# Kernel tuning notes

Hardware: AMD Instinct MI355X
Metric: run time of the kernel (lower is better)

## Reference

```python
import jax, jax.numpy as jnp
import numpy as np

B, N, M = 2, 512, 8192
DIM, CTX, H, DH, MULT = 1024, 512, 16, 64, 4
INNER = H * DH


def layernorm(x, scale, bias, eps=1e-5):
    mu = x.mean(-1, keepdims=True)
    var = ((x - mu) ** 2).mean(-1, keepdims=True)
    return (x - mu) / jnp.sqrt(var + eps) * scale + bias


def rotate_half(x):
    # interleaved pairs: (..., d) -> (..., d/2, 2), (x1, x2) -> (-x2, x1)
    xr = x.reshape(x.shape[:-1] + (-1, 2))
    x1, x2 = xr[..., 0], xr[..., 1]
    return jnp.stack((-x2, x1), axis=-1).reshape(x.shape)


def apply_rope(freqs, x):
    # freqs: [b, seq, dh] -> [b, 1, seq, dh]; x: [b, h, seq, dh]
    f = freqs[:, None, :, :]
    return x * jnp.cos(f) + rotate_half(x) * jnp.sin(f)


def setup_inputs() -> dict:
    key = jax.random.key(0)
    ks = jax.random.split(key, 24)
    s = 0.02
    inp = {
        "x_query": jax.random.normal(ks[0], (B, N, DIM), jnp.float32),
        "x_context": jax.random.normal(ks[1], (B, M, CTX), jnp.float32),
        "rope_q": jax.random.normal(ks[2], (B, N, DH), jnp.float32),
        "rope_ctx": jax.random.normal(ks[3], (B, M, DH), jnp.float32),
        "Wq": jax.random.normal(ks[4], (DIM, INNER), jnp.float32) * s,
        "Wkv": jax.random.normal(ks[5], (CTX, 2 * INNER), jnp.float32) * s,
        "Wo": jax.random.normal(ks[6], (INNER, DIM), jnp.float32) * s,
        "bo": jnp.zeros((DIM,), jnp.float32),
        "ln_q_scale": jnp.ones((DIM,), jnp.float32),
        "ln_q_bias": jnp.zeros((DIM,), jnp.float32),
        "ln_c_scale": jnp.ones((CTX,), jnp.float32),
        "ln_c_bias": jnp.zeros((CTX,), jnp.float32),
        "ffn_ln_scale": jnp.ones((DIM,), jnp.float32),
        "ffn_ln_bias": jnp.zeros((DIM,), jnp.float32),
        "W1": jax.random.normal(ks[7], (DIM, DIM * MULT * 2), jnp.float32) * s,
        "b1": jnp.zeros((DIM * MULT * 2,), jnp.float32),
        "W2": jax.random.normal(ks[8], (DIM * MULT, DIM), jnp.float32) * s,
        "b2": jnp.zeros((DIM,), jnp.float32),
        "attn_mask": jnp.ones((B, M), dtype=bool),
    }
    return inp


def reference(x_query, x_context, rope_q, rope_ctx, Wq, Wkv, Wo, bo,
              ln_q_scale, ln_q_bias, ln_c_scale, ln_c_bias,
              ffn_ln_scale, ffn_ln_bias, W1, b1, W2, b2, attn_mask):
    # --- RotaryCrossAttention ---
    hq = layernorm(x_query, ln_q_scale, ln_q_bias)
    hc = layernorm(x_context, ln_c_scale, ln_c_bias)
    q = (hq @ Wq).reshape(B, N, H, DH).transpose(0, 2, 1, 3)          # b h n d
    kv = hc @ Wkv
    k = kv[..., :INNER].reshape(B, M, H, DH).transpose(0, 2, 1, 3)    # b h m d
    v = kv[..., INNER:].reshape(B, M, H, DH).transpose(0, 2, 1, 3)
    q = apply_rope(rope_q, q)
    k = apply_rope(rope_ctx, k)
    v = apply_rope(rope_ctx, v)  # rotate_value=True
    scale = DH ** -0.5
    scores = jnp.einsum('bhnd,bhmd->bhnm', q, k) * scale
    scores = jnp.where(attn_mask[:, None, None, :], scores, -1e9)
    attn = jax.nn.softmax(scores, axis=-1)
    out = jnp.einsum('bhnm,bhmd->bhnd', attn, v)
    out = apply_rope(-rope_q, out)  # un-rotate values
    out = out.transpose(0, 2, 1, 3).reshape(B, N, INNER)
    out = out @ Wo + bo
    res = x_query + out
    # --- pre-norm GEGLU FeedForward ---
    y = layernorm(res, ffn_ln_scale, ffn_ln_bias)
    u = y @ W1 + b1
    a, g = u[..., :DIM * MULT], u[..., DIM * MULT:]
    z = (a * jax.nn.gelu(g, approximate=False)) @ W2 + b2
    return res + z
```

## Files before the change

### kernel.cpp

```cpp
#include <hip/hip_runtime.h>
#include <hip/hip_bf16.h>
#include <math.h>


typedef __bf16 bf16;
typedef __bf16 bf16x8 __attribute__((ext_vector_type(8)));
typedef float f32x4 __attribute__((ext_vector_type(4)));

#define DEVI static __device__ __forceinline__

union BV {
  uint4 u;
  bf16 b[8];
  bf16x8 v;
};

DEVI float bf2f(bf16 x) { return (float)x; }
DEVI bf16 f2bf(float x) { return (bf16)x; }

DEVI void gload16(const void* g, void* l) {
  __builtin_amdgcn_global_load_lds((const __attribute__((address_space(1))) void*)g,
                                   (__attribute__((address_space(3))) void*)l, 16, 0, 0);
}

template <int EPI>
__global__ __launch_bounds__(256, 2)
void gemm128(const bf16* __restrict__ A, const bf16* __restrict__ Bt,
             int Mdim, int Ndim, int Kdim,
             const float* __restrict__ bias, const float* __restrict__ resid,
             void* __restrict__ out0, void* __restrict__ out1, int sshift) {
  extern __shared__ char smem[];
  bf16* As = (bf16*)smem;
  bf16* Bs = (bf16*)(smem + 16384);
  const int tid = threadIdx.x;
  const int w = tid >> 6, l = tid & 63;
  const int wm = w >> 1, wn = w & 1;
  const int ln15 = l & 15, lh = l >> 4;
  const int sw7 = ln15 & 7;
  int bm, bn;
  if constexpr (EPI == 5) {
    const int fid = blockIdx.x;
    bn = (fid & 7) * 16 + ((fid >> 3) & 15);
    bm = fid >> 7;
  } else {
    bm = blockIdx.x;
    bn = blockIdx.y;
  }
  const int kpz = Kdim / gridDim.z;
  const int kbeg = blockIdx.z * kpz;

  const int srow = w * 32 + (l >> 3);
  const int gcol = ((l & 7) ^ ((l >> 3) & 7)) << 3;
  const bf16* aG = A + (size_t)(bm * 128 + srow) * Kdim + gcol;
  const bf16* bG = Bt + (size_t)(bn * 128 + srow) * Kdim + gcol;
  bf16* lA = As + (w * 32) * 64;
  bf16* lB = Bs + (w * 32) * 64;

  const f32x4 z4 = {0.f, 0.f, 0.f, 0.f};
  f32x4 acc[4][4];
#pragma unroll
  for (int i = 0; i < 4; i++)
#pragma unroll
    for (int j = 0; j < 4; j++) acc[i][j] = z4;

  const char* Ab = (const char*)As;
  const char* Bb = (const char*)Bs;
  const int arow_b = (wm * 64 + ln15) * 128;
  const int brow_b = (wn * 64 + ln15) * 128;

  for (int k0 = kbeg; k0 < kbeg + kpz; k0 += 64) {
#pragma unroll
    for (int gi = 0; gi < 4; gi++) {
      gload16(aG + (size_t)(gi * 8) * Kdim + k0, lA + gi * 512);
      gload16(bG + (size_t)(gi * 8) * Kdim + k0, lB + gi * 512);
    }
    __syncthreads();
#pragma unroll
    for (int kk = 0; kk < 2; kk++) {
      const int gx = (((kk << 2) | lh) ^ sw7) << 4;
      bf16x8 af[4], bfr[4];
#pragma unroll
      for (int f = 0; f < 4; f++) {
        BV t0;
        t0.u = *(const uint4*)(Ab + arow_b + f * 2048 + gx);
        af[f] = t0.v;
        BV t2;
        t2.u = *(const uint4*)(Bb + brow_b + f * 2048 + gx);
        bfr[f] = t2.v;
      }
#pragma unroll
      for (int fm = 0; fm < 4; fm++)
#pragma unroll
        for (int fn = 0; fn < 4; fn++)
          acc[fm][fn] = __builtin_amdgcn_mfma_f32_16x16x32_bf16(af[fm], bfr[fn], acc[fm][fn], 0, 0, 0);
    }
    __syncthreads();
  }

  if constexpr (EPI == 5) {
    const unsigned* cs = (const unsigned*)resid;
    char* ot = smem;
    const bool isK = (bm < 8);
#pragma unroll
    for (int fm = 0; fm < 4; fm++) {
      const int nl0 = wm * 64 + fm * 16 + lh * 4;
#pragma unroll
      for (int fn = 0; fn < 4; fn++) {
        const int ml = wn * 64 + fn * 16 + ln15;
        const int col = bn * 128 + ml;
#pragma unroll
        for (int jp = 0; jp < 2; jp++) {
          const int nl = nl0 + 2 * jp;
          const int d0 = nl & 63;
          const float x0 = acc[fm][fn][2 * jp];
          const float x1 = acc[fm][fn][2 * jp + 1];
          const unsigned cs0 = cs[(size_t)d0 * 16384 + col];
          const unsigned cs1 = cs[(size_t)(d0 + 1) * 16384 + col];
          const float c0 = __uint_as_float(cs0 << 16);
          const float s0 = __uint_as_float(cs0 & 0xffff0000u);
          const float c1 = __uint_as_float(cs1 << 16);
          const float s1 = __uint_as_float(cs1 & 0xffff0000u);
          const float y0 = x0 * c0 - x1 * s0;
          const float y1 = x1 * c1 + x0 * s1;
          if (isK) {
            union { unsigned u; bf16 bb[2]; } pk;
            pk.bb[0] = f2bf(y0);
            pk.bb[1] = f2bf(y1);
            *(unsigned*)(ot + ml * 272 + nl * 2) = pk.u;
          } else {
            *(bf16*)(ot + nl * 272 + ml * 2) = f2bf(y0);
            *(bf16*)(ot + (nl + 1) * 272 + ml * 2) = f2bf(y1);
          }
        }
      }
    }
    __syncthreads();
    const int b = bn >> 6;
    const int mblk = (bn & 63) * 128;
    if (isK) {
#pragma unroll
      for (int it = 0; it < 8; it++) {
        const int id = it * 256 + tid;
        const int hl = id >> 10, rem = id & 1023;
        const int mm = rem >> 3, c = rem & 7;
        const uint4 vv = *(const uint4*)(ot + mm * 272 + hl * 128 + c * 16);
        const int hg = bm * 2 + hl;
        *(uint4*)((bf16*)out0 + ((size_t)(b * 16 + hg) * 8192 + mblk + mm) * 64 + c * 8) = vv;
      }
    } else {
#pragma unroll
      for (int it = 0; it < 8; it++) {
        const int id = it * 256 + tid;
        const int nl = id >> 4, c = id & 15;
        const uint4 vv = *(const uint4*)(ot + nl * 272 + c * 16);
        const int hg = (bm - 8) * 2 + (nl >> 6);
        const int d = nl & 63;
        *(uint4*)((bf16*)out1 + ((size_t)(b * 16 + hg) * 64 + d) * 8192 + mblk + c * 8) = vv;
      }
    }
  } else {
#pragma unroll
    for (int fm = 0; fm < 4; fm++) {
#pragma unroll
      for (int fn = 0; fn < 4; fn++) {
        const int col = bn * 128 + wn * 64 + fn * 16 + ln15;
#pragma unroll
        for (int j = 0; j < 4; j++) {
          const int row = bm * 128 + wm * 64 + fm * 16 + lh * 4 + j;
          if constexpr (EPI == 6) {
            ((bf16*)out0)[((size_t)blockIdx.z * Mdim + row) * Ndim + col] = f2bf(acc[fm][fn][j]);
          } else {
            ((float*)out0)[((size_t)blockIdx.z * Mdim + row) * Ndim + col] = acc[fm][fn][j];
          }
        }
      }
    }
  }
}

__global__ __launch_bounds__(256, 2)
void gemm_geglu(const bf16* __restrict__ A, const bf16* __restrict__ Bt,
                const float* __restrict__ b1, bf16* __restrict__ hg) {
  __shared__ bf16 As[128 * 64];
  __shared__ bf16 Bs[128 * 64];
  const int tid = threadIdx.x;
  const int w = tid >> 6, l = tid & 63;
  const int wm = w >> 1, wn = w & 1;
  const int bm = blockIdx.x, bn = blockIdx.y;
  const int ln15 = l & 15, lh = l >> 4;
  const int sw7 = ln15 & 7;

  const int srow = w * 32 + (l >> 3);
  const int gcol = ((l & 7) ^ ((l >> 3) & 7)) << 3;
  const bf16* aG = A + (size_t)(bm * 128 + srow) * 1024 + gcol;
  const bf16* bG = Bt + (size_t)((w >> 1) * 4096 + bn * 64 + ((w & 1) * 32 + (l >> 3))) * 1024 + gcol;
  bf16* lA = As + (w * 32) * 64;
  bf16* lB = Bs + (w * 32) * 64;

  const f32x4 z4 = {0.f, 0.f, 0.f, 0.f};
  f32x4 acc[2][4][2];
#pragma unroll
  for (int p = 0; p < 2; p++)
#pragma unroll
    for (int i = 0; i < 4; i++)
#pragma unroll
      for (int j = 0; j < 2; j++) acc[p][i][j] = z4;

  const char* Ab = (const char*)As;
  const char* Bb = (const char*)Bs;
  const int arow_b = (wm * 64 + ln15) * 128;

  for (int k0 = 0; k0 < 1024; k0 += 64) {
#pragma unroll
    for (int gi = 0; gi < 4; gi++) {
      gload16(aG + (size_t)(gi * 8) * 1024 + k0, lA + gi * 512);
      gload16(bG + (size_t)(gi * 8) * 1024 + k0, lB + gi * 512);
    }
    __syncthreads();
#pragma unroll
    for (int kk = 0; kk < 2; kk++) {
      const int gx = (((kk << 2) | lh) ^ sw7) << 4;
      bf16x8 af[4], bfr[2][2];
#pragma unroll
      for (int f = 0; f < 4; f++) {
        BV t0;
        t0.u = *(const uint4*)(Ab + arow_b + f * 2048 + gx);
        af[f] = t0.v;
      }
#pragma unroll
      for (int p = 0; p < 2; p++)
#pragma unroll
        for (int fn = 0; fn < 2; fn++) {
          BV t0;
          t0.u = *(const uint4*)(Bb + (p * 64 + wn * 32 + fn * 16 + ln15) * 128 + gx);
          bfr[p][fn] = t0.v;
        }
#pragma unroll
      for (int fm = 0; fm < 4; fm++)
#pragma unroll
        for (int p = 0; p < 2; p++)
#pragma unroll
          for (int fn = 0; fn < 2; fn++)
            acc[p][fm][fn] = __builtin_amdgcn_mfma_f32_16x16x32_bf16(af[fm], bfr[p][fn], acc[p][fm][fn], 0, 0, 0);
    }
    __syncthreads();
  }

#pragma unroll
  for (int fm = 0; fm < 4; fm++) {
#pragma unroll
    for (int fn = 0; fn < 2; fn++) {
      const int cl = bn * 64 + wn * 32 + fn * 16 + ln15;
      const float ba = b1[cl], bg = b1[4096 + cl];
#pragma unroll
      for (int j = 0; j < 4; j++) {
        const int row = bm * 128 + wm * 64 + fm * 16 + lh * 4 + j;
        const float a = acc[0][fm][fn][j] + ba;
        const float g = acc[1][fm][fn][j] + bg;
        const float ge = 0.5f * g * (1.f + erff(g * 0.70710678118f));
        hg[(size_t)row * 4096 + cl] = f2bf(a * ge);
      }
    }
  }
}

template <int S>
__global__ __launch_bounds__(256)
void combine_q_rope(const float* __restrict__ part, const float* __restrict__ ct_,
                    const float* __restrict__ st_, bf16* __restrict__ q_buf) {
  const size_t i4 = ((size_t)blockIdx.x * 256 + threadIdx.x) * 4;
  float4 s = *(const float4*)(part + i4);
#pragma unroll
  for (int p = 1; p < S; p++) {
    const float4 t = *(const float4*)(part + (size_t)p * 1048576 + i4);
    s.x += t.x; s.y += t.y; s.z += t.z; s.w += t.w;
  }
  const int row = (int)(i4 >> 10), col = (int)(i4 & 1023);
  const int h = col >> 6, d = col & 63;
  const int b = row >> 9, n = row & 511;
  const size_t fo = (((size_t)(b << 9) + n) << 6) + d;
  const float4 cv = *(const float4*)(ct_ + fo);
  const float4 sv = *(const float4*)(st_ + fo);
  const float SC = 0.125f * 1.44269504f;
  union { uint2 u; bf16 bb[4]; } o;
  o.bb[0] = f2bf((s.x * cv.x - s.y * sv.x) * SC);
  o.bb[1] = f2bf((s.y * cv.y + s.x * sv.y) * SC);
  o.bb[2] = f2bf((s.z * cv.z - s.w * sv.z) * SC);
  o.bb[3] = f2bf((s.w * cv.w + s.z * sv.w) * SC);
  *(uint2*)(q_buf + ((((size_t)(b * 16 + h)) << 9) + n) * 64 + d) = o.u;
}

template <int S>
__global__ __launch_bounds__(256)
void combine_res_kernel(const float* __restrict__ part, const float* __restrict__ bias,
                        const float* __restrict__ resid, float* __restrict__ out) {
  const size_t i4 = ((size_t)blockIdx.x * 256 + threadIdx.x) * 4;
  float4 s = *(const float4*)(part + i4);
#pragma unroll
  for (int p = 1; p < S; p++) {
    const float4 t = *(const float4*)(part + (size_t)p * 1048576 + i4);
    s.x += t.x; s.y += t.y; s.z += t.z; s.w += t.w;
  }
  const int col = (int)(i4 & 1023);
  const float4 bv = *(const float4*)(bias + col);
  const float4 rv = *(const float4*)(resid + i4);
  s.x += bv.x + rv.x; s.y += bv.y + rv.y; s.z += bv.z + rv.z; s.w += bv.w + rv.w;
  *(float4*)(out + i4) = s;
}

template <int S>
__global__ __launch_bounds__(256)
void combine_res_bf16(const bf16* __restrict__ part, const float* __restrict__ bias,
                      const float* __restrict__ resid, float* __restrict__ out) {
  const size_t i4 = ((size_t)blockIdx.x * 256 + threadIdx.x) * 4;
  float4 s = {0.f, 0.f, 0.f, 0.f};
#pragma unroll
  for (int p = 0; p < S; p++) {
    union { uint2 u; bf16 bb[4]; } t;
    t.u = *(const uint2*)(part + (size_t)p * 1048576 + i4);
    s.x += bf2f(t.bb[0]); s.y += bf2f(t.bb[1]);
    s.z += bf2f(t.bb[2]); s.w += bf2f(t.bb[3]);
  }
  const int col = (int)(i4 & 1023);
  const float4 bv = *(const float4*)(bias + col);
  const float4 rv = *(const float4*)(resid + i4);
  s.x += bv.x + rv.x; s.y += bv.y + rv.y; s.z += bv.z + rv.z; s.w += bv.w + rv.w;
  *(float4*)(out + i4) = s;
}

__global__ __launch_bounds__(256, 4)
void attn_kernel(const bf16* __restrict__ q_buf, const bf16* __restrict__ k_buf,
                 const bf16* __restrict__ v_t, bf16* __restrict__ opart,
                 float* __restrict__ lpart) {
  __shared__ bf16 Ks[2][64 * 64];
  __shared__ bf16 Vs[2][64 * 64];
  __shared__ bf16 Ps[4][16][64];
  const int id = blockIdx.x;
  const int sp = id >> 7, qt = (id >> 5) & 3, bh = id & 31;
  const int tid = threadIdx.x;
  const int w = tid >> 6, l = tid & 63;
  const int ln15 = l & 15, lh = l >> 4;

  const bf16* qbase = q_buf + ((size_t)bh * 512 + qt * 128 + w * 32) * 64;
  const bf16* kbase = k_buf + (size_t)bh * 8192 * 64;
  const bf16* vbase = v_t + (size_t)bh * 64 * 8192;

  bf16x8 aq[2][2];
#pragma unroll
  for (int rh = 0; rh < 2; rh++) {
    const bf16* qp = qbase + (size_t)(rh * 16 + ln15) * 64 + lh * 8;
    BV t0; t0.u = *(const uint4*)qp; aq[rh][0] = t0.v;
    BV t1; t1.u = *(const uint4*)(qp + 32); aq[rh][1] = t1.v;
  }

  const f32x4 z4 = {0.f, 0.f, 0.f, 0.f};
  f32x4 o[2][4];
#pragma unroll
  for (int rh = 0; rh < 2; rh++)
#pragma unroll
    for (int fd = 0; fd < 4; fd++) o[rh][fd] = z4;
  f32x4 ol[2] = {z4, z4};

  BV ones;
#pragma unroll
  for (int i = 0; i < 8; i++) ones.b[i] = f2bf(1.0f);

  const int srow0 = ((w << 1) | 0) * 8 + (l >> 3);
  const int srow1 = ((w << 1) | 1) * 8 + (l >> 3);
  const int slot = l & 7;
  const int g0 = (slot ^ (srow0 & 7)) << 3;
  const int g1 = (slot ^ (srow1 & 7)) << 3;
  const bf16* k0p = kbase + (size_t)srow0 * 64 + g0;
  const bf16* k1p = kbase + (size_t)srow1 * 64 + g1;
  const bf16* v0p = vbase + (size_t)srow0 * 8192 + g0;
  const bf16* v1p = vbase + (size_t)srow1 * 8192 + g1;
  const int lo0 = ((w << 1) | 0) * 512;
  const int lo1 = ((w << 1) | 1) * 512;

  const int mt0 = sp * 16;
  auto STAGE = [&](int b, int mt) {
    const size_t mo = (size_t)mt * 4096;
    const size_t mv = (size_t)mt * 64;
    gload16(k0p + mo, Ks[b] + lo0);
    gload16(k1p + mo, Ks[b] + lo1);
    gload16(v0p + mv, Vs[b] + lo0);
    gload16(v1p + mv, Vs[b] + lo1);
  };

  STAGE(0, mt0);
  __syncthreads();

  char* pbase = (char*)&Ps[w][0][0];
  const int swq = ln15 & 7;

  for (int i = 0; i < 16; i++) {
    const int cur = i & 1;
    if (i < 15) STAGE(cur ^ 1, mt0 + i + 1);

    const char* Kb = (const char*)Ks[cur];
    const char* Vb = (const char*)Vs[cur];

    f32x4 sf[2][4];
#pragma unroll
    for (int rh = 0; rh < 2; rh++)
#pragma unroll
      for (int fn = 0; fn < 4; fn++) sf[rh][fn] = z4;
#pragma unroll
    for (int fn = 0; fn < 4; fn++) {
      const int mrow = fn * 16 + ln15;
      const int sw = mrow & 7;
      BV t0; t0.u = *(const uint4*)(Kb + mrow * 128 + ((lh ^ sw) << 4));
      BV t1; t1.u = *(const uint4*)(Kb + mrow * 128 + (((lh + 4) ^ sw) << 4));
      sf[0][fn] = __builtin_amdgcn_mfma_f32_16x16x32_bf16(t0.v, aq[0][0], sf[0][fn], 0, 0, 0);
      sf[0][fn] = __builtin_amdgcn_mfma_f32_16x16x32_bf16(t1.v, aq[0][1], sf[0][fn], 0, 0, 0);
      sf[1][fn] = __builtin_amdgcn_mfma_f32_16x16x32_bf16(t0.v, aq[1][0], sf[1][fn], 0, 0, 0);
      sf[1][fn] = __builtin_amdgcn_mfma_f32_16x16x32_bf16(t1.v, aq[1][1], sf[1][fn], 0, 0, 0);
    }

    BV pa[2][2];
#pragma unroll
    for (int rh = 0; rh < 2; rh++) {
      char* prow = pbase + ln15 * 128;
#pragma unroll
      for (int fn = 0; fn < 4; fn++) {
        const float p0 = exp2f(sf[rh][fn][0]);
        const float p1 = exp2f(sf[rh][fn][1]);
        const float p2 = exp2f(sf[rh][fn][2]);
        const float p3 = exp2f(sf[rh][fn][3]);
        union { uint2 u; bf16 bb[4]; } pk;
        pk.bb[0] = f2bf(p0); pk.bb[1] = f2bf(p1);
        pk.bb[2] = f2bf(p2); pk.bb[3] = f2bf(p3);
        const int G = (fn * 2 + (lh >> 1)) ^ swq;
        *(uint2*)(prow + G * 16 + (lh & 1) * 8) = pk.u;
      }
#pragma unroll
      for (int mh = 0; mh < 2; mh++) {
        const int R = ((mh << 2) | lh) ^ swq;
        pa[rh][mh].u = *(const uint4*)(pbase + ln15 * 128 + (R << 4));
      }
    }

#pragma unroll
    for (int mh = 0; mh < 2; mh++) {
      ol[0] = __builtin_amdgcn_mfma_f32_16x16x32_bf16(pa[0][mh].v, ones.v, ol[0], 0, 0, 0);
      ol[1] = __builtin_amdgcn_mfma_f32_16x16x32_bf16(pa[1][mh].v, ones.v, ol[1], 0, 0, 0);
#pragma unroll
      for (int fd = 0; fd < 4; fd++) {
        const int drow = fd * 16 + ln15;
        BV bv; bv.u = *(const uint4*)(Vb + drow * 128 + ((((mh << 2) | lh) ^ (drow & 7)) << 4));
        o[0][fd] = __builtin_amdgcn_mfma_f32_16x16x32_bf16(pa[0][mh].v, bv.v, o[0][fd], 0, 0, 0);
        o[1][fd] = __builtin_amdgcn_mfma_f32_16x16x32_bf16(pa[1][mh].v, bv.v, o[1][fd], 0, 0, 0);
      }
    }
    __syncthreads();
  }

#pragma unroll
  for (int rh = 0; rh < 2; rh++) {
    if (ln15 == 0) {
#pragma unroll
      for (int j = 0; j < 4; j++)
        lpart[(size_t)id * 128 + w * 32 + rh * 16 + lh * 4 + j] = ol[rh][j];
    }
    bf16* op = opart + (size_t)id * 8192 + (w * 32 + rh * 16) * 64;
#pragma unroll
    for (int fd = 0; fd < 4; fd++)
#pragma unroll
      for (int j = 0; j < 4; j++)
        op[(lh * 4 + j) * 64 + fd * 16 + ln15] = f2bf(o[rh][fd][j]);
  }
}

__global__ __launch_bounds__(256)
void attn_combine_kernel(const bf16* __restrict__ opart, const float* __restrict__ lpart,
                         const float* __restrict__ ct_, const float* __restrict__ st_,
                         bf16* __restrict__ o_lin) {
  const size_t i4 = ((size_t)blockIdx.x * 256 + threadIdx.x) * 4;
  const int d4 = (int)(i4 & 63);
  const int row = (int)(i4 >> 6);
  const int qg = row & 511;
  const int bh = row >> 9;
  const int qt = qg >> 7, ql = qg & 127;
  const int id0 = (qt << 5) | bh;
  float4 acc = {0.f, 0.f, 0.f, 0.f};
  float L = 0.f;
#pragma unroll
  for (int sp = 0; sp < 8; sp++) {
    const int pid = (sp << 7) | id0;
    union { uint2 u; bf16 bb[4]; } t;
    t.u = *(const uint2*)(opart + (size_t)pid * 8192 + ql * 64 + d4);
    acc.x += bf2f(t.bb[0]); acc.y += bf2f(t.bb[1]);
    acc.z += bf2f(t.bb[2]); acc.w += bf2f(t.bb[3]);
    L += lpart[(size_t)pid * 128 + ql];
  }
  const float inv = 1.f / L;
  const float x0 = acc.x * inv, x1 = acc.y * inv, x2 = acc.z * inv, x3 = acc.w * inv;
  const int b = bh >> 4, h = bh & 15, n = qg;
  const size_t fo = (((size_t)b * 512 + n) * 64) + d4;
  const float4 cv = *(const float4*)(ct_ + fo);
  const float4 sv = *(const float4*)(st_ + fo);
  union { uint2 u; bf16 bb[4]; } o;
  o.bb[0] = f2bf(x0 * cv.x + x1 * sv.x);
  o.bb[1] = f2bf(x1 * cv.y - x0 * sv.y);
  o.bb[2] = f2bf(x2 * cv.z + x3 * sv.z);
  o.bb[3] = f2bf(x3 * cv.w - x2 * sv.w);
  *(uint2*)(o_lin + (((size_t)b * 512 + n) * 1024) + h * 64 + d4) = o.u;
}

template <int W>
DEVI void ln_row(const float* __restrict__ xr, const float* __restrict__ sc,
                 const float* __restrict__ bi, bf16* __restrict__ outr,
                 int tid, float* r0, float* r1) {
  constexpr int PER = W / 256;
  const int w = tid >> 6, l = tid & 63;
  float v[PER];
  if constexpr (PER == 4) {
    const float4 t = *(const float4*)(xr + tid * 4);
    v[0] = t.x; v[1] = t.y; v[2] = t.z; v[3] = t.w;
  } else {
    const float2 t = *(const float2*)(xr + tid * 2);
    v[0] = t.x; v[1] = t.y;
  }
  float s = 0.f, ss = 0.f;
#pragma unroll
  for (int i = 0; i < PER; i++) { s += v[i]; ss += v[i] * v[i]; }
#pragma unroll
  for (int off = 1; off < 64; off <<= 1) { s += __shfl_xor(s, off); ss += __shfl_xor(ss, off); }
  if (l == 0) { r0[w] = s; r1[w] = ss; }
  __syncthreads();
  s = r0[0] + r0[1] + r0[2] + r0[3];
  ss = r1[0] + r1[1] + r1[2] + r1[3];
  const float mu = s * (1.f / W);
  const float rstd = rsqrtf(ss * (1.f / W) - mu * mu + 1e-5f);
  if constexpr (PER == 4) {
    union { uint2 u; bf16 b[4]; } t;
#pragma unroll
    for (int i = 0; i < 4; i++) {
      const int c = tid * 4 + i;
      t.b[i] = f2bf((v[i] - mu) * rstd * sc[c] + bi[c]);
    }
    *(uint2*)(outr + tid * 4) = t.u;
  } else {
    union { unsigned u; bf16 b[2]; } t;
#pragma unroll
    for (int i = 0; i < 2; i++) {
      const int c = tid * 2 + i;
      t.b[i] = f2bf((v[i] - mu) * rstd * sc[c] + bi[c]);
    }
    *(unsigned*)(outr + tid * 2) = t.u;
  }
}

template <int W>
__global__ __launch_bounds__(256)
void ln_kernel(const float* __restrict__ x, const float* __restrict__ sc,
               const float* __restrict__ bi, bf16* __restrict__ out) {
  __shared__ float r0[4], r1[4];
  const int row = blockIdx.x;
  ln_row<W>(x + (size_t)row * W, sc, bi, out + (size_t)row * W, threadIdx.x, r0, r1);
}

__global__ __launch_bounds__(256)
void ln2_kernel(const float* __restrict__ xq, const float* __restrict__ sq,
                const float* __restrict__ bq, bf16* __restrict__ oq,
                const float* __restrict__ xc, const float* __restrict__ sc,
                const float* __restrict__ bc, bf16* __restrict__ oc) {
  __shared__ float r0[4], r1[4];
  const int id = blockIdx.x;
  if (id < 1024) {
    ln_row<1024>(xq + (size_t)id * 1024, sq, bq, oq + (size_t)id * 1024, threadIdx.x, r0, r1);
  } else {
    const int row = id - 1024;
    ln_row<512>(xc + (size_t)row * 512, sc, bc, oc + (size_t)row * 512, threadIdx.x, r0, r1);
  }
}

DEVI void tr_tile(bf16 (*t)[74], const float* __restrict__ in, bf16* __restrict__ out,
                  int R, int C, int ct, int rt, int tid) {
  const int tr = tid >> 2, tc = (tid & 3) << 4;
  {
    const float* src = in + (size_t)(rt * 64 + tr) * C + ct * 64 + tc;
    const float4 a0 = *(const float4*)src;
    const float4 a1 = *(const float4*)(src + 4);
    const float4 a2 = *(const float4*)(src + 8);
    const float4 a3 = *(const float4*)(src + 12);
    t[tr][tc + 0] = f2bf(a0.x);  t[tr][tc + 1] = f2bf(a0.y);
    t[tr][tc + 2] = f2bf(a0.z);  t[tr][tc + 3] = f2bf(a0.w);
    t[tr][tc + 4] = f2bf(a1.x);  t[tr][tc + 5] = f2bf(a1.y);
    t[tr][tc + 6] = f2bf(a1.z);  t[tr][tc + 7] = f2bf(a1.w);
    t[tr][tc + 8] = f2bf(a2.x);  t[tr][tc + 9] = f2bf(a2.y);
    t[tr][tc + 10] = f2bf(a2.z); t[tr][tc + 11] = f2bf(a2.w);
    t[tr][tc + 12] = f2bf(a3.x); t[tr][tc + 13] = f2bf(a3.y);
    t[tr][tc + 14] = f2bf(a3.z); t[tr][tc + 15] = f2bf(a3.w);
  }
  __syncthreads();
  {
    BV a0, a1;
#pragma unroll
    for (int i = 0; i < 8; i++) { a0.b[i] = t[tc + i][tr]; a1.b[i] = t[tc + 8 + i][tr]; }
    bf16* dst = out + (size_t)(ct * 64 + tr) * R + rt * 64 + tc;
    *(uint4*)dst = a0.u;
    *(uint4*)(dst + 8) = a1.u;
  }
}

__global__ __launch_bounds__(256)
void transpose3_kernel(const float* __restrict__ Wq, bf16* __restrict__ WqT,
                       const float* __restrict__ Wkv, bf16* __restrict__ WkvT,
                       const float* __restrict__ Wo, bf16* __restrict__ WoT) {
  __shared__ bf16 t[64][74];
  int id = blockIdx.x;
  if (id < 256) {
    tr_tile(t, Wq, WqT, 1024, 1024, id & 15, id >> 4, threadIdx.x);
  } else if (id < 512) {
    id -= 256;
    tr_tile(t, Wkv, WkvT, 512, 2048, id & 31, id >> 5, threadIdx.x);
  } else {
    id -= 512;
    tr_tile(t, Wo, WoT, 1024, 1024, id & 15, id >> 4, threadIdx.x);
  }
}

__global__ __launch_bounds__(256)
void transpose2_kernel(const float* __restrict__ W1, bf16* __restrict__ W1T,
                       const float* __restrict__ W2, bf16* __restrict__ W2T) {
  __shared__ bf16 t[64][74];
  int id = blockIdx.x;
  if (id < 2048) {
    tr_tile(t, W1, W1T, 1024, 8192, id & 127, id >> 7, threadIdx.x);
  } else {
    id -= 2048;
    tr_tile(t, W2, W2T, 4096, 1024, id & 15, id >> 4, threadIdx.x);
  }
}

__global__ __launch_bounds__(256)
void ropetabs_kernel(const float* __restrict__ fq, float* __restrict__ cq,
                     float* __restrict__ sq, const float* __restrict__ fc,
                     unsigned* __restrict__ cs) {
  const int bid = blockIdx.x;
  if (bid < 256) {
    const int i = bid * 256 + threadIdx.x;
    float sv, cv;
    sincosf(fq[i], &sv, &cv);
    cq[i] = cv;
    sq[i] = sv;
  } else {
    const int i = (bid - 256) * 256 + threadIdx.x;
    float sv, cv;
    sincosf(fc[i], &sv, &cv);
    union { bf16 b; unsigned short u; } cb, sb;
    cb.b = f2bf(cv);
    sb.b = f2bf(sv);
    const int d = i & 63;
    const int bm = i >> 6;
    cs[(size_t)d * 16384 + bm] = ((unsigned)sb.u << 16) | cb.u;
  }
}

extern "C" void kernel_launch(void* const* d_in, const int* in_sizes, int n_in,
                              void* d_out, int out_size, void* d_ws, size_t ws_size,
                              hipStream_t stream) {
  const float* x_query = (const float*)d_in[0];
  const float* x_context = (const float*)d_in[1];
  const float* rope_q = (const float*)d_in[2];
  const float* rope_ctx = (const float*)d_in[3];
  const float* Wq = (const float*)d_in[4];
  const float* Wkv = (const float*)d_in[5];
  const float* Wo = (const float*)d_in[6];
  const float* bo = (const float*)d_in[7];
  const float* lnq_s = (const float*)d_in[8];
  const float* lnq_b = (const float*)d_in[9];
  const float* lnc_s = (const float*)d_in[10];
  const float* lnc_b = (const float*)d_in[11];
  const float* lnf_s = (const float*)d_in[12];
  const float* lnf_b = (const float*)d_in[13];
  const float* W1 = (const float*)d_in[14];
  const float* b1 = (const float*)d_in[15];
  const float* W2 = (const float*)d_in[16];
  const float* b2 = (const float*)d_in[17];

  char* ws = (char*)d_ws;
  size_t off = 0;
  auto alloc = [&](size_t bytes) {
    char* p = ws + off;
    off += (bytes + 255) & ~(size_t)255;
    return p;
  };

  bf16* WqT = (bf16*)alloc((size_t)1048576 * 2);
  bf16* WkvT = (bf16*)alloc((size_t)1048576 * 2);
  bf16* WoT = (bf16*)alloc((size_t)1048576 * 2);
  bf16* hq = (bf16*)alloc((size_t)1048576 * 2);
  bf16* q_buf = (bf16*)alloc((size_t)1048576 * 2);
  float* cosq = (float*)alloc((size_t)65536 * 4);
  float* sinq = (float*)alloc((size_t)65536 * 4);
  unsigned* cs_ctx = (unsigned*)alloc((size_t)1048576 * 4);
  bf16* o_lin = (bf16*)alloc((size_t)1048576 * 2);
  float* res = (float*)alloc((size_t)1048576 * 4);
  bf16* ybuf = (bf16*)alloc((size_t)1048576 * 2);
  float* lpart = (float*)alloc((size_t)131072 * 4);
  bf16* hc = (bf16*)alloc((size_t)8388608 * 2);
  float* pq = (float*)hc;
  bf16* k_buf = (bf16*)alloc((size_t)16777216 * 2);
  bf16* W1T = k_buf;
  bf16* W2T = k_buf + 8388608;
  bf16* hg = k_buf + 8388608 + 4194304;
  char* regB = alloc((size_t)16777216 * 2);
  bf16* opart = (bf16*)regB;
  float* pwo = (float*)regB;
  bf16* pf2 = (bf16*)regB;
  bf16* v_tb = (bf16*)alloc((size_t)16777216 * 2);
  (void)ws_size;

  const int SH = 32768;
  const int SH5 = 34816;

  transpose3_kernel<<<768, 256, 0, stream>>>(Wq, WqT, Wkv, WkvT, Wo, WoT);
  ropetabs_kernel<<<4352, 256, 0, stream>>>(rope_q, cosq, sinq, rope_ctx, cs_ctx);
  ln2_kernel<<<17408, 256, 0, stream>>>(x_query, lnq_s, lnq_b, hq,
                                        x_context, lnc_s, lnc_b, hc);

  gemm128<5><<<2048, 256, SH5, stream>>>(WkvT, hc, 2048, 16384, 512,
                                         nullptr, (const float*)cs_ctx,
                                         k_buf, v_tb, 0);
  gemm128<4><<<dim3(8, 8, 4), 256, SH, stream>>>(hq, WqT, 1024, 1024, 1024, nullptr, nullptr, pq, nullptr, 0);
  combine_q_rope<4><<<1024, 256, 0, stream>>>(pq, cosq, sinq, q_buf);

  attn_kernel<<<1024, 256, 0, stream>>>(q_buf, k_buf, v_tb, opart, lpart);
  attn_combine_kernel<<<1024, 256, 0, stream>>>(opart, lpart, cosq, sinq, o_lin);

  transpose2_kernel<<<3072, 256, 0, stream>>>(W1, W1T, W2, W2T);

  gemm128<4><<<dim3(8, 8, 4), 256, SH, stream>>>(o_lin, WoT, 1024, 1024, 1024, nullptr, nullptr, pwo, nullptr, 0);
  combine_res_kernel<4><<<1024, 256, 0, stream>>>(pwo, bo, x_query, res);

  ln_kernel<1024><<<1024, 256, 0, stream>>>(res, lnf_s, lnf_b, ybuf);
  gemm_geglu<<<dim3(8, 64), 256, 0, stream>>>(ybuf, W1T, b1, hg);
  gemm128<6><<<dim3(8, 8, 8), 256, SH, stream>>>(hg, W2T, 1024, 1024, 4096, nullptr, nullptr, pf2, nullptr, 0);
  combine_res_bf16<8><<<1024, 256, 0, stream>>>(pf2, b2, res, (float*)d_out);
}
```

Measured before the change: 235.3 us.

## Store split-K partials in bf16, fuse residual combine with FFN layernorm, add setprio

```diff
diff --git a/kernel.cpp b/kernel.cpp
--- a/kernel.cpp
+++ b/kernel.cpp
@@ -167,11 +167,7 @@
 #pragma unroll
         for (int j = 0; j < 4; j++) {
           const int row = bm * 128 + wm * 64 + fm * 16 + lh * 4 + j;
-          if constexpr (EPI == 6) {
-            ((bf16*)out0)[((size_t)blockIdx.z * Mdim + row) * Ndim + col] = f2bf(acc[fm][fn][j]);
-          } else {
-            ((float*)out0)[((size_t)blockIdx.z * Mdim + row) * Ndim + col] = acc[fm][fn][j];
-          }
+          ((bf16*)out0)[((size_t)blockIdx.z * Mdim + row) * Ndim + col] = f2bf(acc[fm][fn][j]);
         }
       }
     }
@@ -266,14 +262,16 @@
 
 template <int S>
 __global__ __launch_bounds__(256)
-void combine_q_rope(const float* __restrict__ part, const float* __restrict__ ct_,
+void combine_q_rope(const bf16* __restrict__ part, const float* __restrict__ ct_,
                     const float* __restrict__ st_, bf16* __restrict__ q_buf) {
   const size_t i4 = ((size_t)blockIdx.x * 256 + threadIdx.x) * 4;
-  float4 s = *(const float4*)(part + i4);
-#pragma unroll
-  for (int p = 1; p < S; p++) {
-    const float4 t = *(const float4*)(part + (size_t)p * 1048576 + i4);
-    s.x += t.x; s.y += t.y; s.z += t.z; s.w += t.w;
+  float4 s = {0.f, 0.f, 0.f, 0.f};
+#pragma unroll
+  for (int p = 0; p < S; p++) {
+    union { uint2 u; bf16 bb[4]; } t;
+    t.u = *(const uint2*)(part + (size_t)p * 1048576 + i4);
+    s.x += bf2f(t.bb[0]); s.y += bf2f(t.bb[1]);
+    s.z += bf2f(t.bb[2]); s.w += bf2f(t.bb[3]);
   }
   const int row = (int)(i4 >> 10), col = (int)(i4 & 1023);
   const int h = col >> 6, d = col & 63;
@@ -292,20 +290,45 @@
 
 template <int S>
 __global__ __launch_bounds__(256)
-void combine_res_kernel(const float* __restrict__ part, const float* __restrict__ bias,
-                        const float* __restrict__ resid, float* __restrict__ out) {
-  const size_t i4 = ((size_t)blockIdx.x * 256 + threadIdx.x) * 4;
-  float4 s = *(const float4*)(part + i4);
-#pragma unroll
-  for (int p = 1; p < S; p++) {
-    const float4 t = *(const float4*)(part + (size_t)p * 1048576 + i4);
-    s.x += t.x; s.y += t.y; s.z += t.z; s.w += t.w;
-  }
-  const int col = (int)(i4 & 1023);
+void combine_res_ln(const bf16* __restrict__ part, const float* __restrict__ bias,
+                    const float* __restrict__ resid, float* __restrict__ out,
+                    const float* __restrict__ lnsc, const float* __restrict__ lnbi,
+                    bf16* __restrict__ yout) {
+  __shared__ float r0[4], r1[4];
+  const int row = blockIdx.x, tid = threadIdx.x;
+  const int wv = tid >> 6, l = tid & 63;
+  const size_t i4 = (size_t)row * 1024 + tid * 4;
+  const int col = tid * 4;
+  float4 s = {0.f, 0.f, 0.f, 0.f};
+#pragma unroll
+  for (int p = 0; p < S; p++) {
+    union { uint2 u; bf16 bb[4]; } t;
+    t.u = *(const uint2*)(part + (size_t)p * 1048576 + i4);
+    s.x += bf2f(t.bb[0]); s.y += bf2f(t.bb[1]);
+    s.z += bf2f(t.bb[2]); s.w += bf2f(t.bb[3]);
+  }
   const float4 bv = *(const float4*)(bias + col);
   const float4 rv = *(const float4*)(resid + i4);
   s.x += bv.x + rv.x; s.y += bv.y + rv.y; s.z += bv.z + rv.z; s.w += bv.w + rv.w;
   *(float4*)(out + i4) = s;
+  float sm = s.x + s.y + s.z + s.w;
+  float ss = s.x * s.x + s.y * s.y + s.z * s.z + s.w * s.w;
+#pragma unroll
+  for (int off = 1; off < 64; off <<= 1) { sm += __shfl_xor(sm, off); ss += __shfl_xor(ss, off); }
+  if (l == 0) { r0[wv] = sm; r1[wv] = ss; }
+  __syncthreads();
+  sm = r0[0] + r0[1] + r0[2] + r0[3];
+  ss = r1[0] + r1[1] + r1[2] + r1[3];
+  const float mu = sm * (1.f / 1024.f);
+  const float rstd = rsqrtf(ss * (1.f / 1024.f) - mu * mu + 1e-5f);
+  const float4 scv = *(const float4*)(lnsc + col);
+  const float4 biv = *(const float4*)(lnbi + col);
+  union { uint2 u; bf16 bb[4]; } y;
+  y.bb[0] = f2bf((s.x - mu) * rstd * scv.x + biv.x);
+  y.bb[1] = f2bf((s.y - mu) * rstd * scv.y + biv.y);
+  y.bb[2] = f2bf((s.z - mu) * rstd * scv.z + biv.z);
+  y.bb[3] = f2bf((s.w - mu) * rstd * scv.w + biv.w);
+  *(uint2*)(yout + i4) = y.u;
 }
 
 template <int S>
@@ -405,6 +428,7 @@
     for (int rh = 0; rh < 2; rh++)
 #pragma unroll
       for (int fn = 0; fn < 4; fn++) sf[rh][fn] = z4;
+    __builtin_amdgcn_s_setprio(1);
 #pragma unroll
     for (int fn = 0; fn < 4; fn++) {
       const int mrow = fn * 16 + ln15;
@@ -416,6 +440,7 @@
       sf[1][fn] = __builtin_amdgcn_mfma_f32_16x16x32_bf16(t0.v, aq[1][0], sf[1][fn], 0, 0, 0);
       sf[1][fn] = __builtin_amdgcn_mfma_f32_16x16x32_bf16(t1.v, aq[1][1], sf[1][fn], 0, 0, 0);
     }
+    __builtin_amdgcn_s_setprio(0);
 
     BV pa[2][2];
 #pragma unroll
@@ -440,6 +465,7 @@
       }
     }
 
+    __builtin_amdgcn_s_setprio(1);
 #pragma unroll
     for (int mh = 0; mh < 2; mh++) {
       ol[0] = __builtin_amdgcn_mfma_f32_16x16x32_bf16(pa[0][mh].v, ones.v, ol[0], 0, 0, 0);
@@ -452,6 +478,7 @@
         o[1][fd] = __builtin_amdgcn_mfma_f32_16x16x32_bf16(pa[1][mh].v, bv.v, o[1][fd], 0, 0, 0);
       }
     }
+    __builtin_amdgcn_s_setprio(0);
     __syncthreads();
   }
 
@@ -549,15 +576,6 @@
     }
     *(unsigned*)(outr + tid * 2) = t.u;
   }
-}
-
-template <int W>
-__global__ __launch_bounds__(256)
-void ln_kernel(const float* __restrict__ x, const float* __restrict__ sc,
-               const float* __restrict__ bi, bf16* __restrict__ out) {
-  __shared__ float r0[4], r1[4];
-  const int row = blockIdx.x;
-  ln_row<W>(x + (size_t)row * W, sc, bi, out + (size_t)row * W, threadIdx.x, r0, r1);
 }
 
 __global__ __launch_bounds__(256)
@@ -701,14 +719,14 @@
   bf16* ybuf = (bf16*)alloc((size_t)1048576 * 2);
   float* lpart = (float*)alloc((size_t)131072 * 4);
   bf16* hc = (bf16*)alloc((size_t)8388608 * 2);
-  float* pq = (float*)hc;
+  bf16* pq = hc;
   bf16* k_buf = (bf16*)alloc((size_t)16777216 * 2);
   bf16* W1T = k_buf;
   bf16* W2T = k_buf + 8388608;
   bf16* hg = k_buf + 8388608 + 4194304;
   char* regB = alloc((size_t)16777216 * 2);
   bf16* opart = (bf16*)regB;
-  float* pwo = (float*)regB;
+  bf16* pwo = (bf16*)regB;
   bf16* pf2 = (bf16*)regB;
   bf16* v_tb = (bf16*)alloc((size_t)16777216 * 2);
   (void)ws_size;
@@ -724,7 +742,7 @@
   gemm128<5><<<2048, 256, SH5, stream>>>(WkvT, hc, 2048, 16384, 512,
                                          nullptr, (const float*)cs_ctx,
                                          k_buf, v_tb, 0);
-  gemm128<4><<<dim3(8, 8, 4), 256, SH, stream>>>(hq, WqT, 1024, 1024, 1024, nullptr, nullptr, pq, nullptr, 0);
+  gemm128<6><<<dim3(8, 8, 4), 256, SH, stream>>>(hq, WqT, 1024, 1024, 1024, nullptr, nullptr, pq, nullptr, 0);
   combine_q_rope<4><<<1024, 256, 0, stream>>>(pq, cosq, sinq, q_buf);
 
   attn_kernel<<<1024, 256, 0, stream>>>(q_buf, k_buf, v_tb, opart, lpart);
@@ -732,10 +750,9 @@
 
   transpose2_kernel<<<3072, 256, 0, stream>>>(W1, W1T, W2, W2T);
 
-  gemm128<4><<<dim3(8, 8, 4), 256, SH, stream>>>(o_lin, WoT, 1024, 1024, 1024, nullptr, nullptr, pwo, nullptr, 0);
-  combine_res_kernel<4><<<1024, 256, 0, stream>>>(pwo, bo, x_query, res);
-
-  ln_kernel<1024><<<1024, 256, 0, stream>>>(res, lnf_s, lnf_b, ybuf);
+  gemm128<6><<<dim3(8, 8, 4), 256, SH, stream>>>(o_lin, WoT, 1024, 1024, 1024, nullptr, nullptr, pwo, nullptr, 0);
+  combine_res_ln<4><<<1024, 256, 0, stream>>>(pwo, bo, x_query, res, lnf_s, lnf_b, ybuf);
+
   gemm_geglu<<<dim3(8, 64), 256, 0, stream>>>(ybuf, W1T, b1, hg);
   gemm128<6><<<dim3(8, 8, 8), 256, SH, stream>>>(hg, W2T, 1024, 1024, 4096, nullptr, nullptr, pf2, nullptr, 0);
   combine_res_bf16<8><<<1024, 256, 0, stream>>>(pf2, b2, res, (float*)d_out);
```

Result: faster. 228.6 us (-2.9%).
